# Kernel optimization log

Hardware: AMD Instinct MI355X
Metric: run time of the kernel (lower is better)

The kernel has to match this reference:

```python
import jax, jax.numpy as jnp
import numpy as np
import math

D_MODEL = 1024
N_HEAD = 16
NEG = -1e10  # matches torch masked_fill value

def setup_inputs() -> dict:
    key = jax.random.key(0)
    ks = jax.random.split(key, 5)
    B, S, D = 2, 2048, D_MODEL
    s = 0.02
    return {
        "x": jax.random.normal(ks[0], (B, S, D), jnp.float32),
        "w_qkv": jax.random.normal(ks[1], (3 * D, D), jnp.float32) * s,  # torch Linear weight [out,in]
        "b_qkv": jnp.zeros((3 * D,), jnp.float32),
        "w_out": jax.random.normal(ks[2], (D, D), jnp.float32) * s,
        "b_out": jnp.zeros((D,), jnp.float32),
    }

def reference(x, w_qkv, b_qkv, w_out, b_out):
    B, S, D = x.shape
    H = N_HEAD
    dk = D // H
    qkv = x @ w_qkv.T + b_qkv                      # [B,S,3D]
    q, k, v = jnp.split(qkv, 3, axis=2)
    def heads(t):
        return t.reshape(B, S, H, dk).transpose(0, 2, 1, 3)  # [B,H,S,dk]
    q, k, v = heads(q), heads(k), heads(v)
    scores = jnp.einsum('bhqd,bhkd->bhqk', q, k) / math.sqrt(dk)
    mask = jnp.tril(jnp.ones((S, S), bool))
    scores = jnp.where(mask, scores, NEG)
    attn = jax.nn.softmax(scores, axis=-1)
    out = jnp.einsum('bhqk,bhkd->bhqd', attn, v)   # [B,H,S,dk]
    out = out.transpose(0, 2, 1, 3).reshape(B, S, D)
    return out @ w_out.T + b_out
```

## Files before the change

kernel.cpp:

```cpp
#include <hip/hip_runtime.h>

typedef __attribute__((ext_vector_type(8))) short short8;
typedef __attribute__((ext_vector_type(4))) float floatx4;

#define DMODEL 1024
#define NHEAD  16
#define DK     64
#define SEQ    2048
#define QSCALE 0.18033688011112042f

__device__ __forceinline__ unsigned short f2bf(float f) {
  unsigned u = __builtin_bit_cast(unsigned, f);
  u += 0x7FFF + ((u >> 16) & 1);
  return (unsigned short)(u >> 16);
}

__global__ void f2bf_kernel(const float* __restrict__ in, unsigned short* __restrict__ out, int n4) {
  int i = blockIdx.x * 256 + threadIdx.x;
  int stride = gridDim.x * 256;
  for (; i < n4; i += stride) {
    float4 v = reinterpret_cast<const float4*>(in)[i];
    ushort4 o;
    o.x = f2bf(v.x); o.y = f2bf(v.y); o.z = f2bf(v.z); o.w = f2bf(v.w);
    reinterpret_cast<ushort4*>(out)[i] = o;
  }
}

__device__ __forceinline__ void gload16(const void* g, void* l) {
  __builtin_amdgcn_global_load_lds((const __attribute__((address_space(1))) void*)g,
                                   (__attribute__((address_space(3))) void*)l, 16, 0, 0);
}

template<int MODE>
__global__ __launch_bounds__(256)
void gemm_bt(const unsigned short* __restrict__ A, const unsigned short* __restrict__ Bt,
             const float* __restrict__ bias, float* __restrict__ Cf,
             unsigned short* __restrict__ Qo, unsigned short* __restrict__ Ko,
             unsigned short* __restrict__ Vro, int M, int N, int K)
{
  __shared__ short Al[2][128 * 32];
  __shared__ short Bl[2][128 * 32];
  const int tid = threadIdx.x, lane = tid & 63, wave = tid >> 6;
  const int wr = wave >> 1, wc = wave & 1;
  const int m0 = blockIdx.x * 128, n0 = blockIdx.y * 128;

  floatx4 z4 = {0.f, 0.f, 0.f, 0.f};
  floatx4 acc[4][4];
#pragma unroll
  for (int i = 0; i < 4; i++)
#pragma unroll
    for (int j = 0; j < 4; j++) acc[i][j] = z4;

  auto STAGE = [&](int sb, int k0) {
#pragma unroll
    for (int i = 0; i < 2; i++) {
      int chunk = wave * 2 + i;
      int e = chunk * 512 + lane * 8;
      int row = e >> 5, kc = e & 31;
      gload16(A  + (size_t)(m0 + row) * K + k0 + kc, &Al[sb][chunk * 512]);
      gload16(Bt + (size_t)(n0 + row) * K + k0 + kc, &Bl[sb][chunk * 512]);
    }
  };

  STAGE(0, 0);
  int buf = 0;
  for (int k0 = 0; k0 < K; k0 += 32) {
    __syncthreads();
    if (k0 + 32 < K) STAGE(buf ^ 1, k0 + 32);
    const short* Ac = Al[buf];
    const short* Bc = Bl[buf];
    short8 af[4], bfr[4];
#pragma unroll
    for (int i = 0; i < 4; i++) {
      af[i]  = *reinterpret_cast<const short8*>(&Ac[(wr * 64 + i * 16 + (lane & 15)) * 32 + ((lane >> 4) << 3)]);
      bfr[i] = *reinterpret_cast<const short8*>(&Bc[(wc * 64 + i * 16 + (lane & 15)) * 32 + ((lane >> 4) << 3)]);
    }
#pragma unroll
    for (int i = 0; i < 4; i++)
#pragma unroll
      for (int j = 0; j < 4; j++)
        acc[i][j] = __builtin_amdgcn_mfma_f32_16x16x32_bf16(af[i], bfr[j], acc[i][j], 0, 0, 0);
    buf ^= 1;
  }

#pragma unroll
  for (int i = 0; i < 4; i++) {
#pragma unroll
    for (int j = 0; j < 4; j++) {
#pragma unroll
      for (int r = 0; r < 4; r++) {
        int m = m0 + wr * 64 + i * 16 + ((lane >> 4) << 2) + r;
        int n = n0 + wc * 64 + j * 16 + (lane & 15);
        float v = acc[i][j][r] + bias[n];
        if (MODE == 1) {
          Cf[(size_t)m * N + n] = v;
        } else {
          int which = n >> 10;
          int h = (n & 1023) >> 6;
          int d = n & 63;
          int b = m >> 11, s = m & 2047;
          int bh = (b << 4) + h;
          size_t idx = ((size_t)bh * SEQ + s) * DK + d;
          if (which == 0)      Qo[idx]  = f2bf(v * QSCALE);
          else if (which == 1) Ko[idx]  = f2bf(v);
          else                 Vro[idx] = f2bf(v);
        }
      }
    }
  }
}

__global__ __launch_bounds__(256)
void transpose_v(const unsigned short* __restrict__ Vr, unsigned short* __restrict__ Vt) {
  __shared__ unsigned short T[64][68];
  const int tid = threadIdx.x;
  const int bh = blockIdx.x, st = blockIdx.y;
  const int s0 = st * 64;
  const unsigned short* src = Vr + ((size_t)bh * SEQ + s0) * DK;
#pragma unroll
  for (int i = 0; i < 4; i++) {
    int idx = tid + 256 * i;
    int row = idx >> 4, c = (idx & 15) << 2;
    ushort4 v = *reinterpret_cast<const ushort4*>(&src[row * DK + c]);
    *reinterpret_cast<ushort4*>(&T[row][c]) = v;
  }
  __syncthreads();
  unsigned short* dst = Vt + (size_t)bh * DK * SEQ + s0;
#pragma unroll
  for (int i = 0; i < 4; i++) {
    int idx = tid + 256 * i;
    int d = idx >> 4, sc = (idx & 15) << 2;
    ushort4 o;
    o.x = T[sc + 0][d]; o.y = T[sc + 1][d]; o.z = T[sc + 2][d]; o.w = T[sc + 3][d];
    *reinterpret_cast<ushort4*>(&dst[(size_t)d * SEQ + sc]) = o;
  }
}

__global__ __launch_bounds__(512)
void attn_kernel(const unsigned short* __restrict__ Qb, const unsigned short* __restrict__ Kb,
                 const unsigned short* __restrict__ Vtb, unsigned short* __restrict__ AO)
{
  __shared__ short Kl[2][4096];
  __shared__ short Vl[2][4096];
  __shared__ short Pl[8][1024];
  const int tid = threadIdx.x, lane = tid & 63, wave = tid >> 6;
  const int bh = blockIdx.x;
  const int y = blockIdx.y;
  const int qt = (y < 8) ? y : (23 - y);
  const int b = bh >> 4, h = bh & 15;
  const int q0 = qt * 128;
  const int qrow_w = q0 + wave * 16;
  const int qlast = qrow_w + 15;
  const unsigned short* Qh = Qb  + (size_t)bh * SEQ * DK;
  const unsigned short* Kh = Kb  + (size_t)bh * SEQ * DK;
  const unsigned short* Vh = Vtb + (size_t)bh * DK * SEQ;
  short* Pw = Pl[wave];

  short8 qf[2];
  {
    int arow = qrow_w + (lane & 15);
#pragma unroll
    for (int ks = 0; ks < 2; ks++)
      qf[ks] = *reinterpret_cast<const short8*>(&Qh[(size_t)arow * DK + ks * 32 + ((lane >> 4) << 3)]);
  }

  floatx4 z4 = {0.f, 0.f, 0.f, 0.f};
  floatx4 o[4];
  float m_[4], l_[4];
#pragma unroll
  for (int db = 0; db < 4; db++) o[db] = z4;
#pragma unroll
  for (int r = 0; r < 4; r++) { m_[r] = -1e30f; l_[r] = 0.f; }

  const int srow = lane >> 3;
  const int srk  = ((lane & 7) ^ srow) << 3;
  auto STAGE = [&](int sb, int kv0) {
    int row = wave * 8 + srow;
    gload16(Kh + (size_t)(kv0 + row) * DK + srk, &Kl[sb][wave * 512]);
    gload16(Vh + (size_t)row * SEQ + kv0 + srk,  &Vl[sb][wave * 512]);
  };

  const int ntiles = 2 * qt + 2;
  STAGE(0, 0);
  int buf = 0;
  for (int it = 0; it < ntiles; it++) {
    __syncthreads();
    if (it + 1 < ntiles) STAGE(buf ^ 1, (it + 1) * 64);
    const short* Kc = Kl[buf];
    const short* Vc = Vl[buf];
    buf ^= 1;
    const int kv0 = it * 64;
    if (kv0 > qlast) continue;

    const bool masked = (kv0 + 63 > qrow_w);

    floatx4 sc[4];
#pragma unroll
    for (int nb = 0; nb < 4; nb++) sc[nb] = z4;
#pragma unroll
    for (int ks = 0; ks < 2; ks++) {
#pragma unroll
      for (int nb = 0; nb < 4; nb++) {
        int kvr = nb * 16 + (lane & 15);
        short8 kf = *reinterpret_cast<const short8*>(
            &Kc[((kvr << 6) + ks * 32 + ((lane >> 4) << 3)) ^ ((kvr & 7) << 3)]);
        sc[nb] = __builtin_amdgcn_mfma_f32_16x16x32_bf16(qf[ks], kf, sc[nb], 0, 0, 0);
      }
    }

    float sv[4][4];
    const int lrb = (lane >> 4) << 2;
#pragma unroll
    for (int nb = 0; nb < 4; nb++)
#pragma unroll
      for (int r = 0; r < 4; r++) sv[nb][r] = sc[nb][r];
    if (masked) {
      int kvb = kv0 + (lane & 15);
      int qr = qrow_w + lrb;
#pragma unroll
      for (int nb = 0; nb < 4; nb++)
#pragma unroll
        for (int r = 0; r < 4; r++)
          sv[nb][r] = (kvb + nb * 16 <= qr + r) ? sv[nb][r] : -1e30f;
    }
    float mx4[4] = {-1e30f, -1e30f, -1e30f, -1e30f};
#pragma unroll
    for (int nb = 0; nb < 4; nb++)
#pragma unroll
      for (int r = 0; r < 4; r++) mx4[r] = fmaxf(mx4[r], sv[nb][r]);
#pragma unroll
    for (int msk = 1; msk < 16; msk <<= 1)
#pragma unroll
      for (int r = 0; r < 4; r++) mx4[r] = fmaxf(mx4[r], __shfl_xor(mx4[r], msk));

    float nm[4]; bool need = false;
#pragma unroll
    for (int r = 0; r < 4; r++) { nm[r] = fmaxf(m_[r], mx4[r]); need = need || (nm[r] - m_[r] > 8.0f); }
    if (__any(need)) {
#pragma unroll
      for (int r = 0; r < 4; r++) {
        float al = __builtin_amdgcn_exp2f(m_[r] - nm[r]);
        m_[r] = nm[r];
        l_[r] *= al;
#pragma unroll
        for (int db = 0; db < 4; db++) o[db][r] *= al;
      }
    }

    float rs4[4] = {0.f, 0.f, 0.f, 0.f};
#pragma unroll
    for (int nb = 0; nb < 4; nb++)
#pragma unroll
      for (int r = 0; r < 4; r++) {
        float p = __builtin_amdgcn_exp2f(sv[nb][r] - m_[r]);
        unsigned pu = __builtin_bit_cast(unsigned, p);
        rs4[r] += __builtin_bit_cast(float, pu & 0xffff0000u);
        int lr = lrb + r;
        Pw[((lr << 6) + nb * 16 + (lane & 15)) ^ ((lr & 7) << 3)] = (short)(pu >> 16);
      }
#pragma unroll
    for (int msk = 1; msk < 16; msk <<= 1)
#pragma unroll
      for (int r = 0; r < 4; r++) rs4[r] += __shfl_xor(rs4[r], msk);
#pragma unroll
    for (int r = 0; r < 4; r++) l_[r] += rs4[r];

#pragma unroll
    for (int ks2 = 0; ks2 < 2; ks2++) {
      int lr = lane & 15;
      short8 pf = *reinterpret_cast<const short8*>(
          &Pw[((lr << 6) + ks2 * 32 + ((lane >> 4) << 3)) ^ ((lr & 7) << 3)]);
#pragma unroll
      for (int db = 0; db < 4; db++) {
        int dr = db * 16 + (lane & 15);
        short8 vf = *reinterpret_cast<const short8*>(
            &Vc[((dr << 6) + ks2 * 32 + ((lane >> 4) << 3)) ^ ((dr & 7) << 3)]);
        o[db] = __builtin_amdgcn_mfma_f32_16x16x32_bf16(pf, vf, o[db], 0, 0, 0);
      }
    }
  }

  float rl[4];
#pragma unroll
  for (int r = 0; r < 4; r++) rl[r] = __builtin_amdgcn_rcpf(l_[r]);
  const int lrb = (lane >> 4) << 2;
#pragma unroll
  for (int db = 0; db < 4; db++) {
#pragma unroll
    for (int r = 0; r < 4; r++) {
      int q = qrow_w + lrb + r;
      int d = db * 16 + (lane & 15);
      AO[((size_t)(b * SEQ + q)) * DMODEL + h * DK + d] = f2bf(o[db][r] * rl[r]);
    }
  }
}

extern "C" void kernel_launch(void* const* d_in, const int* in_sizes, int n_in,
                              void* d_out, int out_size, void* d_ws, size_t ws_size,
                              hipStream_t stream) {
  (void)in_sizes; (void)n_in; (void)out_size; (void)ws_size;
  const float* x     = (const float*)d_in[0];
  const float* w_qkv = (const float*)d_in[1];
  const float* b_qkv = (const float*)d_in[2];
  const float* w_out = (const float*)d_in[3];
  const float* b_out = (const float*)d_in[4];
  float* out = (float*)d_out;

  char* ws = (char*)d_ws;
  unsigned short* xb    = (unsigned short*)(ws);
  unsigned short* wqkvb = (unsigned short*)(ws + (8u  << 20));
  unsigned short* woutb = (unsigned short*)(ws + (14u << 20));
  unsigned short* Qb    = (unsigned short*)(ws + (16u << 20));
  unsigned short* Kb    = (unsigned short*)(ws + (24u << 20));
  unsigned short* Vrow  = (unsigned short*)(ws + (32u << 20));
  unsigned short* Vtb   = (unsigned short*)(ws + (40u << 20));
  unsigned short* AOb   = xb;

  f2bf_kernel<<<2048, 256, 0, stream>>>(x,     xb,    4194304 / 4);
  f2bf_kernel<<<2048, 256, 0, stream>>>(w_qkv, wqkvb, 3145728 / 4);
  f2bf_kernel<<<1024, 256, 0, stream>>>(w_out, woutb, 1048576 / 4);

  gemm_bt<0><<<dim3(32, 24), 256, 0, stream>>>(xb, wqkvb, b_qkv, nullptr,
                                               Qb, Kb, Vrow, 4096, 3072, 1024);

  transpose_v<<<dim3(32, 32), 256, 0, stream>>>(Vrow, Vtb);

  attn_kernel<<<dim3(32, 16), 512, 0, stream>>>(Qb, Kb, Vtb, AOb);

  gemm_bt<1><<<dim3(32, 8), 256, 0, stream>>>(AOb, woutb, b_out, out,
                                              nullptr, nullptr, nullptr, 4096, 1024, 1024);
}
```

Baseline: 211.8 us.

## Fuse f2bf launches, shrink attention and out-projection tiles for more blocks

Merges the three fp32-to-bf16 conversion launches into one kernel. The attention kernel moves from 128-row query tiles with 8 waves to 64-row tiles with 4 waves, launching 1024 blocks and dropping the paired load-balancing index. Row-sum reduction is deferred until after the PV MFMAs and now sums unrounded probabilities. A dedicated output-projection GEMM uses 64x128 tiles to double the block count. Together these aim to cut launch overhead and improve CU occupancy, at the cost of reloading K/V more often in attention and a slight numeric change in normalization.

```diff
diff --git a/kernel.cpp b/kernel.cpp
--- a/kernel.cpp
+++ b/kernel.cpp
@@ -15,14 +15,24 @@
   return (unsigned short)(u >> 16);
 }
 
-__global__ void f2bf_kernel(const float* __restrict__ in, unsigned short* __restrict__ out, int n4) {
+__global__ void f2bf_all(const float* __restrict__ x, const float* __restrict__ wq,
+                         const float* __restrict__ wo,
+                         unsigned short* __restrict__ xb, unsigned short* __restrict__ wqb,
+                         unsigned short* __restrict__ wob) {
+  const int n1 = 1048576;
+  const int n2 = 786432;
+  const int n3 = 262144;
   int i = blockIdx.x * 256 + threadIdx.x;
   int stride = gridDim.x * 256;
-  for (; i < n4; i += stride) {
-    float4 v = reinterpret_cast<const float4*>(in)[i];
+  for (; i < n1 + n2 + n3; i += stride) {
+    const float* src; unsigned short* dst; int j;
+    if (i < n1)            { src = x;  dst = xb;  j = i; }
+    else if (i < n1 + n2)  { src = wq; dst = wqb; j = i - n1; }
+    else                   { src = wo; dst = wob; j = i - n1 - n2; }
+    float4 v = reinterpret_cast<const float4*>(src)[j];
     ushort4 o;
     o.x = f2bf(v.x); o.y = f2bf(v.y); o.z = f2bf(v.z); o.w = f2bf(v.w);
-    reinterpret_cast<ushort4*>(out)[i] = o;
+    reinterpret_cast<ushort4*>(dst)[j] = o;
   }
 }
 
@@ -31,13 +41,12 @@
                                    (__attribute__((address_space(3))) void*)l, 16, 0, 0);
 }
 
-template<int MODE>
 __global__ __launch_bounds__(256)
-void gemm_bt(const unsigned short* __restrict__ A, const unsigned short* __restrict__ Bt,
-             const float* __restrict__ bias, float* __restrict__ Cf,
-             unsigned short* __restrict__ Qo, unsigned short* __restrict__ Ko,
-             unsigned short* __restrict__ Vro, int M, int N, int K)
-{
+void gemm_qkv(const unsigned short* __restrict__ A, const unsigned short* __restrict__ Bt,
+              const float* __restrict__ bias,
+              unsigned short* __restrict__ Qo, unsigned short* __restrict__ Ko,
+              unsigned short* __restrict__ Vro) {
+  const int K = DMODEL;
   __shared__ short Al[2][128 * 32];
   __shared__ short Bl[2][128 * 32];
   const int tid = threadIdx.x, lane = tid & 63, wave = tid >> 6;
@@ -92,19 +101,15 @@
         int m = m0 + wr * 64 + i * 16 + ((lane >> 4) << 2) + r;
         int n = n0 + wc * 64 + j * 16 + (lane & 15);
         float v = acc[i][j][r] + bias[n];
-        if (MODE == 1) {
-          Cf[(size_t)m * N + n] = v;
-        } else {
-          int which = n >> 10;
-          int h = (n & 1023) >> 6;
-          int d = n & 63;
-          int b = m >> 11, s = m & 2047;
-          int bh = (b << 4) + h;
-          size_t idx = ((size_t)bh * SEQ + s) * DK + d;
-          if (which == 0)      Qo[idx]  = f2bf(v * QSCALE);
-          else if (which == 1) Ko[idx]  = f2bf(v);
-          else                 Vro[idx] = f2bf(v);
-        }
+        int which = n >> 10;
+        int h = (n & 1023) >> 6;
+        int d = n & 63;
+        int b = m >> 11, s = m & 2047;
+        int bh = (b << 4) + h;
+        size_t idx = ((size_t)bh * SEQ + s) * DK + d;
+        if (which == 0)      Qo[idx]  = f2bf(v * QSCALE);
+        else if (which == 1) Ko[idx]  = f2bf(v);
+        else                 Vro[idx] = f2bf(v);
       }
     }
   }
@@ -136,25 +141,23 @@
   }
 }
 
-__global__ __launch_bounds__(512)
+__global__ __launch_bounds__(256)
 void attn_kernel(const unsigned short* __restrict__ Qb, const unsigned short* __restrict__ Kb,
                  const unsigned short* __restrict__ Vtb, unsigned short* __restrict__ AO)
 {
   __shared__ short Kl[2][4096];
   __shared__ short Vl[2][4096];
-  __shared__ short Pl[8][1024];
+  __shared__ short Pl[4][1024];
   const int tid = threadIdx.x, lane = tid & 63, wave = tid >> 6;
-  const int bh = blockIdx.x;
-  const int y = blockIdx.y;
-  const int qt = (y < 8) ? y : (23 - y);
+  const int bh = blockIdx.x, qt = blockIdx.y;
   const int b = bh >> 4, h = bh & 15;
-  const int q0 = qt * 128;
+  const int q0 = qt * 64;
   const int qrow_w = q0 + wave * 16;
-  const int qlast = qrow_w + 15;
   const unsigned short* Qh = Qb  + (size_t)bh * SEQ * DK;
   const unsigned short* Kh = Kb  + (size_t)bh * SEQ * DK;
   const unsigned short* Vh = Vtb + (size_t)bh * DK * SEQ;
   short* Pw = Pl[wave];
+  const int lrb = (lane >> 4) << 2;
 
   short8 qf[2];
   {
@@ -175,12 +178,15 @@
   const int srow = lane >> 3;
   const int srk  = ((lane & 7) ^ srow) << 3;
   auto STAGE = [&](int sb, int kv0) {
-    int row = wave * 8 + srow;
-    gload16(Kh + (size_t)(kv0 + row) * DK + srk, &Kl[sb][wave * 512]);
-    gload16(Vh + (size_t)row * SEQ + kv0 + srk,  &Vl[sb][wave * 512]);
+#pragma unroll
+    for (int sub = 0; sub < 2; sub++) {
+      int row = wave * 16 + sub * 8 + srow;
+      gload16(Kh + (size_t)(kv0 + row) * DK + srk, &Kl[sb][wave * 1024 + sub * 512]);
+      gload16(Vh + (size_t)row * SEQ + kv0 + srk,  &Vl[sb][wave * 1024 + sub * 512]);
+    }
   };
 
-  const int ntiles = 2 * qt + 2;
+  const int ntiles = qt + 1;
   STAGE(0, 0);
   int buf = 0;
   for (int it = 0; it < ntiles; it++) {
@@ -190,8 +196,6 @@
     const short* Vc = Vl[buf];
     buf ^= 1;
     const int kv0 = it * 64;
-    if (kv0 > qlast) continue;
-
     const bool masked = (kv0 + 63 > qrow_w);
 
     floatx4 sc[4];
@@ -208,12 +212,6 @@
       }
     }
 
-    float sv[4][4];
-    const int lrb = (lane >> 4) << 2;
-#pragma unroll
-    for (int nb = 0; nb < 4; nb++)
-#pragma unroll
-      for (int r = 0; r < 4; r++) sv[nb][r] = sc[nb][r];
     if (masked) {
       int kvb = kv0 + (lane & 15);
       int qr = qrow_w + lrb;
@@ -221,13 +219,13 @@
       for (int nb = 0; nb < 4; nb++)
 #pragma unroll
         for (int r = 0; r < 4; r++)
-          sv[nb][r] = (kvb + nb * 16 <= qr + r) ? sv[nb][r] : -1e30f;
+          sc[nb][r] = (kvb + nb * 16 <= qr + r) ? sc[nb][r] : -1e30f;
     }
     float mx4[4] = {-1e30f, -1e30f, -1e30f, -1e30f};
 #pragma unroll
     for (int nb = 0; nb < 4; nb++)
 #pragma unroll
-      for (int r = 0; r < 4; r++) mx4[r] = fmaxf(mx4[r], sv[nb][r]);
+      for (int r = 0; r < 4; r++) mx4[r] = fmaxf(mx4[r], sc[nb][r]);
 #pragma unroll
     for (int msk = 1; msk < 16; msk <<= 1)
 #pragma unroll
@@ -252,18 +250,12 @@
     for (int nb = 0; nb < 4; nb++)
 #pragma unroll
       for (int r = 0; r < 4; r++) {
-        float p = __builtin_amdgcn_exp2f(sv[nb][r] - m_[r]);
-        unsigned pu = __builtin_bit_cast(unsigned, p);
-        rs4[r] += __builtin_bit_cast(float, pu & 0xffff0000u);
+        float p = __builtin_amdgcn_exp2f(sc[nb][r] - m_[r]);
+        rs4[r] += p;
         int lr = lrb + r;
-        Pw[((lr << 6) + nb * 16 + (lane & 15)) ^ ((lr & 7) << 3)] = (short)(pu >> 16);
-      }
-#pragma unroll
-    for (int msk = 1; msk < 16; msk <<= 1)
-#pragma unroll
-      for (int r = 0; r < 4; r++) rs4[r] += __shfl_xor(rs4[r], msk);
-#pragma unroll
-    for (int r = 0; r < 4; r++) l_[r] += rs4[r];
+        Pw[((lr << 6) + nb * 16 + (lane & 15)) ^ ((lr & 7) << 3)] =
+            (short)(__builtin_bit_cast(unsigned, p) >> 16);
+      }
 
 #pragma unroll
     for (int ks2 = 0; ks2 < 2; ks2++) {
@@ -278,12 +270,18 @@
         o[db] = __builtin_amdgcn_mfma_f32_16x16x32_bf16(pf, vf, o[db], 0, 0, 0);
       }
     }
+
+#pragma unroll
+    for (int msk = 1; msk < 16; msk <<= 1)
+#pragma unroll
+      for (int r = 0; r < 4; r++) rs4[r] += __shfl_xor(rs4[r], msk);
+#pragma unroll
+    for (int r = 0; r < 4; r++) l_[r] += rs4[r];
   }
 
   float rl[4];
 #pragma unroll
   for (int r = 0; r < 4; r++) rl[r] = __builtin_amdgcn_rcpf(l_[r]);
-  const int lrb = (lane >> 4) << 2;
 #pragma unroll
   for (int db = 0; db < 4; db++) {
 #pragma unroll
@@ -293,6 +291,72 @@
       AO[((size_t)(b * SEQ + q)) * DMODEL + h * DK + d] = f2bf(o[db][r] * rl[r]);
     }
   }
+}
+
+__global__ __launch_bounds__(256)
+void gemm_out(const unsigned short* __restrict__ A, const unsigned short* __restrict__ Bt,
+              const float* __restrict__ bias, float* __restrict__ Cf) {
+  const int K = DMODEL, N = DMODEL;
+  __shared__ short Al[2][64 * 32];
+  __shared__ short Bl[2][128 * 32];
+  const int tid = threadIdx.x, lane = tid & 63, wave = tid >> 6;
+  const int wr = wave >> 1, wc = wave & 1;
+  const int m0 = blockIdx.x * 64, n0 = blockIdx.y * 128;
+
+  floatx4 z4 = {0.f, 0.f, 0.f, 0.f};
+  floatx4 acc[2][4];
+#pragma unroll
+  for (int i = 0; i < 2; i++)
+#pragma unroll
+    for (int j = 0; j < 4; j++) acc[i][j] = z4;
+
+  auto STAGE = [&](int sb, int k0) {
+    {
+      int e = wave * 512 + lane * 8;
+      int row = e >> 5, kc = e & 31;
+      gload16(A + (size_t)(m0 + row) * K + k0 + kc, &Al[sb][wave * 512]);
+    }
+#pragma unroll
+    for (int i = 0; i < 2; i++) {
+      int chunk = wave * 2 + i;
+      int e = chunk * 512 + lane * 8;
+      int row = e >> 5, kc = e & 31;
+      gload16(Bt + (size_t)(n0 + row) * K + k0 + kc, &Bl[sb][chunk * 512]);
+    }
+  };
+
+  STAGE(0, 0);
+  int buf = 0;
+  for (int k0 = 0; k0 < K; k0 += 32) {
+    __syncthreads();
+    if (k0 + 32 < K) STAGE(buf ^ 1, k0 + 32);
+    const short* Ac = Al[buf];
+    const short* Bc = Bl[buf];
+    short8 af[2], bfr[4];
+#pragma unroll
+    for (int i = 0; i < 2; i++)
+      af[i]  = *reinterpret_cast<const short8*>(&Ac[(wr * 32 + i * 16 + (lane & 15)) * 32 + ((lane >> 4) << 3)]);
+#pragma unroll
+    for (int j = 0; j < 4; j++)
+      bfr[j] = *reinterpret_cast<const short8*>(&Bc[(wc * 64 + j * 16 + (lane & 15)) * 32 + ((lane >> 4) << 3)]);
+#pragma unroll
+    for (int i = 0; i < 2; i++)
+#pragma unroll
+      for (int j = 0; j < 4; j++)
+        acc[i][j] = __builtin_amdgcn_mfma_f32_16x16x32_bf16(af[i], bfr[j], acc[i][j], 0, 0, 0);
+    buf ^= 1;
+  }
+
+#pragma unroll
+  for (int i = 0; i < 2; i++)
+#pragma unroll
+    for (int j = 0; j < 4; j++)
+#pragma unroll
+      for (int r = 0; r < 4; r++) {
+        int m = m0 + wr * 32 + i * 16 + ((lane >> 4) << 2) + r;
+        int n = n0 + wc * 64 + j * 16 + (lane & 15);
+        Cf[(size_t)m * N + n] = acc[i][j][r] + bias[n];
+      }
 }
 
 extern "C" void kernel_launch(void* const* d_in, const int* in_sizes, int n_in,
@@ -316,17 +380,13 @@
   unsigned short* Vtb   = (unsigned short*)(ws + (40u << 20));
   unsigned short* AOb   = xb;
 
-  f2bf_kernel<<<2048, 256, 0, stream>>>(x,     xb,    4194304 / 4);
-  f2bf_kernel<<<2048, 256, 0, stream>>>(w_qkv, wqkvb, 3145728 / 4);
-  f2bf_kernel<<<1024, 256, 0, stream>>>(w_out, woutb, 1048576 / 4);
-
-  gemm_bt<0><<<dim3(32, 24), 256, 0, stream>>>(xb, wqkvb, b_qkv, nullptr,
-                                               Qb, Kb, Vrow, 4096, 3072, 1024);
+  f2bf_all<<<2048, 256, 0, stream>>>(x, w_qkv, w_out, xb, wqkvb, woutb);
+
+  gemm_qkv<<<dim3(32, 24), 256, 0, stream>>>(xb, wqkvb, b_qkv, Qb, Kb, Vrow);
 
   transpose_v<<<dim3(32, 32), 256, 0, stream>>>(Vrow, Vtb);
 
-  attn_kernel<<<dim3(32, 16), 512, 0, stream>>>(Qb, Kb, Vtb, AOb);
-
-  gemm_bt<1><<<dim3(32, 8), 256, 0, stream>>>(AOb, woutb, b_out, out,
-                                              nullptr, nullptr, nullptr, 4096, 1024, 1024);
-}
+  attn_kernel<<<dim3(32, 32), 256, 0, stream>>>(Qb, Kb, Vtb, AOb);
+
+  gemm_out<<<dim3(64, 8), 256, 0, stream>>>(AOb, woutb, b_out, out);
+}
```

After: 222.3 us. 1.05x slower.
